# Kernel tuning notes

Hardware: AMD Instinct MI355X
Metric: run time of the kernel (lower is better)

## Reference

```python
import jax, jax.numpy as jnp
import numpy as np

N_NODES = 100000
N_EDGES = 3200000
IN_F = 256
OUT_F = 256
NEG_SLOPE = 0.2


def setup_inputs() -> dict:
    key = jax.random.key(0)
    ks = jax.random.split(key, 8)
    x = jax.random.normal(ks[0], (N_NODES, IN_F), dtype=jnp.float32)
    # linear_v: in_features -> out_features (W stored [in, out], y = x @ W + b)
    Wv = jax.random.normal(ks[1], (IN_F, OUT_F), dtype=jnp.float32) / np.sqrt(IN_F)
    bv = jnp.zeros((OUT_F,), dtype=jnp.float32)
    # linear_q / linear_k: out_features -> 1 (stored as vectors)
    wq = jax.random.normal(ks[2], (OUT_F,), dtype=jnp.float32) / np.sqrt(OUT_F)
    bq = jnp.zeros((), dtype=jnp.float32)
    wk = jax.random.normal(ks[3], (OUT_F,), dtype=jnp.float32) / np.sqrt(OUT_F)
    bk = jnp.zeros((), dtype=jnp.float32)
    src = jax.random.randint(ks[4], (N_EDGES,), 0, N_NODES, dtype=jnp.int32)
    dst = jax.random.randint(ks[5], (N_EDGES,), 0, N_NODES, dtype=jnp.int32)
    return {"x": x, "Wv": Wv, "bv": bv, "wq": wq, "bq": bq,
            "wk": wk, "bk": bk, "src": src, "dst": dst}


def reference(x, Wv, bv, wq, bq, wk, bk, src, dst):
    n = x.shape[0]
    h = x @ Wv + bv                      # [N, OUT_F] node values 'u'
    q = h @ wq + bq                      # [N] scalar per node
    k = h @ wk + bk                      # [N]
    e = q[src] + k[dst]                  # [E] u_add_v
    c = jnp.where(e > 0, e, NEG_SLOPE * e)  # leaky relu
    # edge softmax over incoming edges of each dst node (numerically stable)
    m = jax.ops.segment_max(c, dst, num_segments=n)   # [N]
    ex = jnp.exp(c - m[dst])                          # [E]
    s = jax.ops.segment_sum(ex, dst, num_segments=n)  # [N]
    attn = ex / s[dst]                                # [E]
    msg = h[src] * attn[:, None]                      # [E, OUT_F] u_mul_e
    out = jax.ops.segment_sum(msg, dst, num_segments=n)  # [N, OUT_F]
    return out
```

## Files before the change

kernel.cpp:

```cpp
#include <hip/hip_runtime.h>
#include <hip/hip_bf16.h>
#include <stdint.h>

#define NN 100000
#define NE 3200000
#define NPAD 100096
#define NB 391
#define CAPB 12288
#define SCAP 9216
#define GBLK 196
#define EPB 16384

typedef float  f32x4 __attribute__((ext_vector_type(4)));
typedef float  f32x2 __attribute__((ext_vector_type(2)));
typedef short  bf16x8 __attribute__((ext_vector_type(8)));
typedef int    i32x4 __attribute__((ext_vector_type(4)));

__device__ __forceinline__ float bf2f(unsigned short u){
  union { unsigned int i; float f; } v; v.i = ((unsigned int)u) << 16; return v.f;
}
__device__ __forceinline__ unsigned short f2bf(float f){
  __hip_bfloat16 b = __float2bfloat16(f);
  return __builtin_bit_cast(unsigned short, b);
}

__global__ __launch_bounds__(256) void k_prep_wvt(const float* __restrict__ Wv,
                                                  unsigned short* __restrict__ wvt){
  int n = blockIdx.x;
  int kp = threadIdx.x;
  int seg = kp >> 6, ct = (kp >> 3) & 7, o = kp & 7;
  int ks = (seg << 6) | ((ct ^ (n & 7)) << 3) | o;
  wvt[n * 256 + kp] = f2bf(Wv[ks * 256 + n]);
}

__global__ __launch_bounds__(256) void k_prep_vq(const float* __restrict__ Wv,
    const float* __restrict__ bv, const float* __restrict__ wq, const float* __restrict__ bq,
    const float* __restrict__ wk, const float* __restrict__ bk,
    float* __restrict__ vq, float* __restrict__ vk, float* __restrict__ consts){
  __shared__ float red[8];
  __shared__ float red2[8];
  int k = blockIdx.x, n = threadIdx.x;
  int wid = n >> 6, lane = n & 63;
  float w = Wv[k * 256 + n];
  float s1 = w * wq[n], s2 = w * wk[n];
  #pragma unroll
  for (int o = 32; o; o >>= 1){ s1 += __shfl_xor(s1, o, 64); s2 += __shfl_xor(s2, o, 64); }
  if (lane == 0){ red[wid] = s1; red[4 + wid] = s2; }
  __syncthreads();
  if (n == 0){ vq[k] = red[0]+red[1]+red[2]+red[3]; vk[k] = red[4]+red[5]+red[6]+red[7]; }
  if (k == 0){
    float t1 = bv[n] * wq[n], t2 = bv[n] * wk[n];
    #pragma unroll
    for (int o = 32; o; o >>= 1){ t1 += __shfl_xor(t1, o, 64); t2 += __shfl_xor(t2, o, 64); }
    if (lane == 0){ red2[wid] = t1; red2[4 + wid] = t2; }
    __syncthreads();
    if (n == 0){
      consts[0] = red2[0]+red2[1]+red2[2]+red2[3] + bq[0];
      consts[1] = red2[4]+red2[5]+red2[6]+red2[7] + bk[0];
    }
  }
}

__global__ __launch_bounds__(256) void k_convert_qk(const float* __restrict__ x,
    const float* __restrict__ vq, const float* __restrict__ vk, const float* __restrict__ consts,
    unsigned short* __restrict__ xs, float* __restrict__ q, float* __restrict__ kv){
  int row = (blockIdx.x * 256 + threadIdx.x) >> 6;
  int lane = threadIdx.x & 63;
  f32x4 xv = *(const f32x4*)(x + (size_t)row * 256 + lane * 4);
  f32x4 a  = *(const f32x4*)(vq + lane * 4);
  f32x4 b  = *(const f32x4*)(vk + lane * 4);
  float s1 = xv[0]*a[0] + xv[1]*a[1] + xv[2]*a[2] + xv[3]*a[3];
  float s2 = xv[0]*b[0] + xv[1]*b[1] + xv[2]*b[2] + xv[3]*b[3];
  ushort4 v4;
  v4.x = f2bf(xv[0]); v4.y = f2bf(xv[1]); v4.z = f2bf(xv[2]); v4.w = f2bf(xv[3]);
  int ct = ((lane >> 1) & 7) ^ (row & 7);
  char* dst = (char*)xs + (size_t)row * 512 + (lane >> 4) * 128 + ct * 16 + (lane & 1) * 8;
  *(ushort4*)dst = v4;
  #pragma unroll
  for (int o = 32; o; o >>= 1){ s1 += __shfl_xor(s1, o, 64); s2 += __shfl_xor(s2, o, 64); }
  if (lane == 0){ q[row] = s1 + consts[0]; kv[row] = s2 + consts[1]; }
}

__global__ __launch_bounds__(256) void k_gemm(const unsigned short* __restrict__ xs,
    const unsigned short* __restrict__ wvt, const float* __restrict__ bv,
    unsigned short* __restrict__ h){
  __shared__ unsigned short As[128 * 64];
  __shared__ unsigned short Bs[128 * 64];
  int bid = blockIdx.x;
  int bm = bid >> 1, bn = bid & 1;
  int tid = threadIdx.x, wid = tid >> 6, lane = tid & 63;
  int wr = wid >> 1, wc = wid & 1;
  f32x4 zero = {0.f, 0.f, 0.f, 0.f};
  f32x4 acc[4][4];
  #pragma unroll
  for (int i = 0; i < 4; i++)
    #pragma unroll
    for (int j = 0; j < 4; j++) acc[i][j] = zero;
  const char* gA0 = (const char*)xs  + (size_t)bm * 128 * 512;
  const char* gB0 = (const char*)wvt + (size_t)bn * 128 * 512;
  for (int k0b = 0; k0b < 512; k0b += 128){
    #pragma unroll
    for (int it = 0; it < 4; ++it){
      int base = (wid * 4 + it) * 1024;
      int loff = base + lane * 16;
      int row = loff >> 7, cb = loff & 127;
      __builtin_amdgcn_global_load_lds(
        (const __attribute__((address_space(1))) void*)(gA0 + (size_t)row * 512 + k0b + cb),
        (__attribute__((address_space(3))) void*)((char*)As + base), 16, 0, 0);
      __builtin_amdgcn_global_load_lds(
        (const __attribute__((address_space(1))) void*)(gB0 + (size_t)row * 512 + k0b + cb),
        (__attribute__((address_space(3))) void*)((char*)Bs + base), 16, 0, 0);
    }
    __syncthreads();
    #pragma unroll
    for (int kk = 0; kk < 2; ++kk){
      bf16x8 af[4], bfr[4];
      int cbase = kk * 4 + (lane >> 4);
      #pragma unroll
      for (int m = 0; m < 4; m++){
        int row = wr * 64 + m * 16 + (lane & 15);
        int c = cbase ^ (row & 7);
        af[m] = *(const bf16x8*)(As + row * 64 + c * 8);
      }
      #pragma unroll
      for (int n = 0; n < 4; n++){
        int col = wc * 64 + n * 16 + (lane & 15);
        int c = cbase ^ (col & 7);
        bfr[n] = *(const bf16x8*)(Bs + col * 64 + c * 8);
      }
      #pragma unroll
      for (int m = 0; m < 4; m++)
        #pragma unroll
        for (int n = 0; n < 4; n++)
          acc[m][n] = __builtin_amdgcn_mfma_f32_16x16x32_bf16(af[m], bfr[n], acc[m][n], 0, 0, 0);
    }
    __syncthreads();
  }
  unsigned short* hh = h + (size_t)bn * NPAD * 128;
  float bvv[4];
  #pragma unroll
  for (int n = 0; n < 4; n++) bvv[n] = bv[bn * 128 + wc * 64 + n * 16 + (lane & 15)];
  #pragma unroll
  for (int m = 0; m < 4; m++){
    int rowb = bm * 128 + wr * 64 + m * 16 + (lane >> 4) * 4;
    #pragma unroll
    for (int n = 0; n < 4; n++){
      int hcol = wc * 64 + n * 16 + (lane & 15);
      #pragma unroll
      for (int i = 0; i < 4; i++)
        hh[(size_t)(rowb + i) * 128 + hcol] = f2bf(acc[m][n][i] + bvv[n]);
    }
  }
}

__global__ __launch_bounds__(256) void k_group(const int* __restrict__ src,
    const int* __restrict__ dst, int* __restrict__ gTail, int* __restrict__ gReal,
    unsigned int* __restrict__ binned){
  __shared__ unsigned int   raw[EPB];
  __shared__ unsigned short rawB[EPB];
  __shared__ int cnt[NB];
  __shared__ int base[NB];
  __shared__ int cnt2[NB];
  int tid = threadIdx.x;
  for (int b = tid; b < NB; b += 256){ cnt[b] = 0; cnt2[b] = 0; }
  __syncthreads();
  int e0 = blockIdx.x * EPB;
  for (int r = 0; r < 16; ++r){
    int ebase = e0 + r * 1024 + tid * 4;
    int slot  = r * 1024 + tid * 4;
    uint4 vv; ushort4 bb4;
    if (ebase + 3 < NE){
      i32x4 s4 = __builtin_nontemporal_load((const i32x4*)(src + ebase));
      i32x4 d4 = __builtin_nontemporal_load((const i32x4*)(dst + ebase));
      #pragma unroll
      for (int j = 0; j < 4; j++){
        int d = d4[j]; int bkt = d >> 8;
        ((unsigned int*)&vv)[j] = ((unsigned)s4[j] << 8) | (unsigned)(d & 255);
        ((unsigned short*)&bb4)[j] = (unsigned short)bkt;
        atomicAdd(&cnt[bkt], 1);
      }
    } else {
      #pragma unroll
      for (int j = 0; j < 4; j++){
        int e = ebase + j;
        if (e < NE){
          int d = dst[e]; int s = src[e]; int bkt = d >> 8;
          ((unsigned int*)&vv)[j] = ((unsigned)s << 8) | (unsigned)(d & 255);
          ((unsigned short*)&bb4)[j] = (unsigned short)bkt;
          atomicAdd(&cnt[bkt], 1);
        } else {
          ((unsigned int*)&vv)[j] = 0xFFFFFFFFu;
          ((unsigned short*)&bb4)[j] = 0xFFFFu;
        }
      }
    }
    *(uint4*)(raw + slot) = vv;
    *(ushort4*)(rawB + slot) = bb4;
  }
  __syncthreads();
  for (int b = tid; b < NB; b += 256){
    int rr = cnt[b];
    int pr = (rr + 15) & ~15;
    int bs = atomicAdd(&gTail[b], pr);
    base[b] = bs;
    if (rr) atomicAdd(&gReal[b], rr);
    unsigned int* dp = binned + (size_t)b * CAPB;
    for (int k2 = rr; k2 < pr; ++k2){
      int p = bs + k2;
      if (p < CAPB) dp[p] = 0xFFFFFFFFu;
    }
  }
  __syncthreads();
  for (int r = 0; r < 16; ++r){
    int slot = r * 1024 + tid * 4;
    uint4 vv = *(const uint4*)(raw + slot);
    ushort4 bb4 = *(const ushort4*)(rawB + slot);
    #pragma unroll
    for (int j = 0; j < 4; j++){
      unsigned short bkt = ((unsigned short*)&bb4)[j];
      if (bkt != 0xFFFFu){
        int p = base[bkt] + atomicAdd(&cnt2[bkt], 1);
        if (p < CAPB) binned[(size_t)bkt * CAPB + p] = ((unsigned int*)&vv)[j];
      }
    }
  }
}

__global__ __launch_bounds__(256) void k_scanB(const int* __restrict__ gReal,
                                               int* __restrict__ bucketBase){
  __shared__ int sd[512];
  int tid = threadIdx.x;
  int v0 = tid < NB ? gReal[tid] : 0;
  int v1 = (tid + 256) < NB ? gReal[tid + 256] : 0;
  sd[tid] = v0; sd[tid + 256] = v1;
  __syncthreads();
  for (int o = 1; o < 512; o <<= 1){
    int t0 = (tid >= o) ? sd[tid - o] : 0;
    int t1 = (tid + 256 >= o) ? sd[tid + 256 - o] : 0;
    __syncthreads();
    sd[tid] += t0; sd[tid + 256] += t1;
    __syncthreads();
  }
  if (tid < NB) bucketBase[tid] = sd[tid] - v0;
  if (tid + 256 < NB) bucketBase[tid + 256] = sd[tid + 256] - v1;
}

__global__ __launch_bounds__(256) void k_sort(const unsigned int* __restrict__ binned,
    const int* __restrict__ gTail, const int* __restrict__ bucketBase,
    int* __restrict__ deg, int* __restrict__ rowStart, int* __restrict__ csrSrc){
  __shared__ int cnt[256], excl[256], cur[256];
  __shared__ int sorted[SCAP];
  int b = blockIdx.x, tid = threadIdx.x;
  int n = gTail[b]; if (n > CAPB) n = CAPB;
  int base = bucketBase[b];
  const unsigned int* L = binned + (size_t)b * CAPB;
  cnt[tid] = 0;
  __syncthreads();
  for (int i = tid; i < n; i += 256){
    unsigned int v = __builtin_nontemporal_load(L + i);
    if ((v >> 8) < NN) atomicAdd(&cnt[v & 255], 1);
  }
  __syncthreads();
  int myc = cnt[tid];
  excl[tid] = myc;
  __syncthreads();
  for (int o = 1; o < 256; o <<= 1){
    int t = (tid >= o) ? excl[tid - o] : 0;
    __syncthreads();
    excl[tid] += t;
    __syncthreads();
  }
  int ex = excl[tid] - myc;
  int node = b * 256 + tid;
  if (node < NN){ deg[node] = myc; rowStart[node] = base + ex; }
  cur[tid] = ex;
  __syncthreads();
  int m = excl[255];
  for (int i = tid; i < n; i += 256){
    unsigned int v = __builtin_nontemporal_load(L + i);
    unsigned int s = v >> 8;
    if (s < NN){
      int p = atomicAdd(&cur[v & 255], 1);
      if (p < SCAP) sorted[p] = (int)s;
    }
  }
  __syncthreads();
  for (int i = tid; i < m; i += 256)
    __builtin_nontemporal_store(sorted[i], csrSrc + base + i);
}

__global__ __launch_bounds__(256) void k_agg(const int* __restrict__ csrSrc,
    const int* __restrict__ rowStart, const int* __restrict__ deg,
    const float* __restrict__ q, const float* __restrict__ kv,
    const unsigned short* __restrict__ hh, float* __restrict__ outp){
  int w = (blockIdx.x * 256 + threadIdx.x) >> 6;
  int lane = threadIdx.x & 63;
  int start = rowStart[w], d = deg[w];
  float kd = kv[w];
  float a0 = 0.f, a1 = 0.f, ssum = 0.f;
  for (int bse = 0; bse < d; bse += 64){
    int cnt = min(64, d - bse);
    float ex = 0.f; int s = 0;
    if (lane < cnt){
      s = __builtin_nontemporal_load(csrSrc + start + bse + lane);
      float c = q[s] + kd;
      c = c > 0.f ? c : 0.2f * c;
      ex = __expf(c);
    }
    ssum += ex;
    for (int j0 = 0; j0 < cnt; j0 += 8){
      float wg[8]; ushort2 hv[8];
      #pragma unroll
      for (int jj = 0; jj < 8; jj++){
        int j = j0 + jj;
        wg[jj] = __shfl(ex, j, 64);
        int sj = __shfl(s, j, 64);
        hv[jj] = *(const ushort2*)(hh + (size_t)sj * 128 + lane * 2);
      }
      #pragma unroll
      for (int jj = 0; jj < 8; jj++){
        a0 += wg[jj] * bf2f(hv[jj].x);
        a1 += wg[jj] * bf2f(hv[jj].y);
      }
    }
  }
  #pragma unroll
  for (int o = 32; o; o >>= 1) ssum += __shfl_xor(ssum, o, 64);
  float inv = d > 0 ? 1.0f / ssum : 0.0f;
  f32x2 r; r[0] = a0 * inv; r[1] = a1 * inv;
  __builtin_nontemporal_store(r, (f32x2*)(outp + (size_t)w * 256 + lane * 2));
}

extern "C" void kernel_launch(void* const* d_in, const int* in_sizes, int n_in,
                              void* d_out, int out_size, void* d_ws, size_t ws_size,
                              hipStream_t stream){
  const float* x  = (const float*)d_in[0];
  const float* Wv = (const float*)d_in[1];
  const float* bv = (const float*)d_in[2];
  const float* wq = (const float*)d_in[3];
  const float* bq = (const float*)d_in[4];
  const float* wk = (const float*)d_in[5];
  const float* bk = (const float*)d_in[6];
  const int*   src = (const int*)d_in[7];
  const int*   dst = (const int*)d_in[8];
  float* out = (float*)d_out;

  char* ws = (char*)d_ws;
  size_t off = 0;
  auto alloc = [&](size_t bytes) -> char* {
    off = (off + 511) & ~(size_t)511;
    char* p = ws + off; off += bytes; return p;
  };
  unsigned short* h  = (unsigned short*)alloc((size_t)NPAD * 256 * 2);
  unsigned short* xs = (unsigned short*)alloc((size_t)NPAD * 256 * 2);
  unsigned int* binned = (unsigned int*)xs;
  int* csrSrc = (int*)((char*)xs + (size_t)NB * CAPB * 4);
  unsigned short* wvt  = (unsigned short*)alloc(256 * 256 * 2);
  float* vq     = (float*)alloc(256 * 4);
  float* vk     = (float*)alloc(256 * 4);
  float* consts = (float*)alloc(512);
  float* q      = (float*)alloc((size_t)NN * 4);
  float* kv     = (float*)alloc((size_t)NN * 4);
  int* deg      = (int*)alloc((size_t)NN * 4);
  int* rowStart = (int*)alloc((size_t)NN * 4);
  int* gTail    = (int*)alloc((size_t)NB * 4 * 2);
  int* gReal    = gTail + NB;
  int* bucketBase = (int*)alloc((size_t)NB * 4);

  (void)hipMemsetAsync(gTail, 0, (size_t)NB * 4 * 2, stream);
  k_prep_wvt<<<256, 256, 0, stream>>>(Wv, wvt);
  k_prep_vq<<<256, 256, 0, stream>>>(Wv, bv, wq, bq, wk, bk, vq, vk, consts);
  k_convert_qk<<<NN / 4, 256, 0, stream>>>(x, vq, vk, consts, xs, q, kv);
  k_gemm<<<(NPAD / 128) * 2, 256, 0, stream>>>(xs, wvt, bv, h);
  k_group<<<GBLK, 256, 0, stream>>>(src, dst, gTail, gReal, binned);
  k_scanB<<<1, 256, 0, stream>>>(gReal, bucketBase);
  k_sort<<<NB, 256, 0, stream>>>(binned, gTail, bucketBase, deg, rowStart, csrSrc);
  k_agg<<<NN / 4, 256, 0, stream>>>(csrSrc, rowStart, deg, q, kv, h, out);
  k_agg<<<NN / 4, 256, 0, stream>>>(csrSrc, rowStart, deg, q, kv,
                                    h + (size_t)NPAD * 128, out + 128);
}
```

Baseline: 515.4 us.

## Aggregate all 256 features in one pass and fold small kernels together

The h matrix is now stored as a single row-major [N,256] bf16 array instead of two 128-column halves. k_agg processes all 256 columns in one launch, with each lane loading 4 bf16 values and writing a float4, so the per-edge softmax weight work and the CSR/q reads happen once instead of twice. The two prep kernels are merged into one launch, and the bucket scan is recomputed redundantly inside each k_sort block, removing two launches. The trade-off is lower occupancy or memory-level parallelism per edge in k_agg, plus redundant scan work in every sort block.

```diff
diff --git a/kernel.cpp b/kernel.cpp
--- a/kernel.cpp
+++ b/kernel.cpp
@@ -12,34 +12,30 @@
 #define EPB 16384
 
 typedef float  f32x4 __attribute__((ext_vector_type(4)));
-typedef float  f32x2 __attribute__((ext_vector_type(2)));
 typedef short  bf16x8 __attribute__((ext_vector_type(8)));
 typedef int    i32x4 __attribute__((ext_vector_type(4)));
 
-__device__ __forceinline__ float bf2f(unsigned short u){
-  union { unsigned int i; float f; } v; v.i = ((unsigned int)u) << 16; return v.f;
-}
 __device__ __forceinline__ unsigned short f2bf(float f){
   __hip_bfloat16 b = __float2bfloat16(f);
   return __builtin_bit_cast(unsigned short, b);
 }
 
-__global__ __launch_bounds__(256) void k_prep_wvt(const float* __restrict__ Wv,
-                                                  unsigned short* __restrict__ wvt){
-  int n = blockIdx.x;
-  int kp = threadIdx.x;
-  int seg = kp >> 6, ct = (kp >> 3) & 7, o = kp & 7;
-  int ks = (seg << 6) | ((ct ^ (n & 7)) << 3) | o;
-  wvt[n * 256 + kp] = f2bf(Wv[ks * 256 + n]);
-}
-
-__global__ __launch_bounds__(256) void k_prep_vq(const float* __restrict__ Wv,
+__global__ __launch_bounds__(256) void k_prep(const float* __restrict__ Wv,
     const float* __restrict__ bv, const float* __restrict__ wq, const float* __restrict__ bq,
     const float* __restrict__ wk, const float* __restrict__ bk,
-    float* __restrict__ vq, float* __restrict__ vk, float* __restrict__ consts){
+    unsigned short* __restrict__ wvt, float* __restrict__ vq, float* __restrict__ vk,
+    float* __restrict__ consts){
   __shared__ float red[8];
   __shared__ float red2[8];
-  int k = blockIdx.x, n = threadIdx.x;
+  if (blockIdx.x < 256){
+    int n = blockIdx.x;
+    int kp = threadIdx.x;
+    int seg = kp >> 6, ct = (kp >> 3) & 7, o = kp & 7;
+    int ks = (seg << 6) | ((ct ^ (n & 7)) << 3) | o;
+    wvt[n * 256 + kp] = f2bf(Wv[ks * 256 + n]);
+    return;
+  }
+  int k = blockIdx.x - 256, n = threadIdx.x;
   int wid = n >> 6, lane = n & 63;
   float w = Wv[k * 256 + n];
   float s1 = w * wq[n], s2 = w * wk[n];
@@ -136,19 +132,19 @@
     }
     __syncthreads();
   }
-  unsigned short* hh = h + (size_t)bn * NPAD * 128;
+  int colb = bn * 128 + wc * 64;
   float bvv[4];
   #pragma unroll
-  for (int n = 0; n < 4; n++) bvv[n] = bv[bn * 128 + wc * 64 + n * 16 + (lane & 15)];
+  for (int n = 0; n < 4; n++) bvv[n] = bv[colb + n * 16 + (lane & 15)];
   #pragma unroll
   for (int m = 0; m < 4; m++){
     int rowb = bm * 128 + wr * 64 + m * 16 + (lane >> 4) * 4;
     #pragma unroll
     for (int n = 0; n < 4; n++){
-      int hcol = wc * 64 + n * 16 + (lane & 15);
+      int col = colb + n * 16 + (lane & 15);
       #pragma unroll
       for (int i = 0; i < 4; i++)
-        hh[(size_t)(rowb + i) * 128 + hcol] = f2bf(acc[m][n][i] + bvv[n]);
+        h[(size_t)(rowb + i) * 256 + col] = f2bf(acc[m][n][i] + bvv[n]);
     }
   }
 }
@@ -226,36 +222,28 @@
   }
 }
 
-__global__ __launch_bounds__(256) void k_scanB(const int* __restrict__ gReal,
-                                               int* __restrict__ bucketBase){
-  __shared__ int sd[512];
-  int tid = threadIdx.x;
-  int v0 = tid < NB ? gReal[tid] : 0;
-  int v1 = (tid + 256) < NB ? gReal[tid + 256] : 0;
-  sd[tid] = v0; sd[tid + 256] = v1;
-  __syncthreads();
-  for (int o = 1; o < 512; o <<= 1){
-    int t0 = (tid >= o) ? sd[tid - o] : 0;
-    int t1 = (tid + 256 >= o) ? sd[tid + 256 - o] : 0;
-    __syncthreads();
-    sd[tid] += t0; sd[tid + 256] += t1;
-    __syncthreads();
-  }
-  if (tid < NB) bucketBase[tid] = sd[tid] - v0;
-  if (tid + 256 < NB) bucketBase[tid + 256] = sd[tid + 256] - v1;
-}
-
 __global__ __launch_bounds__(256) void k_sort(const unsigned int* __restrict__ binned,
-    const int* __restrict__ gTail, const int* __restrict__ bucketBase,
+    const int* __restrict__ gTail, const int* __restrict__ gReal,
     int* __restrict__ deg, int* __restrict__ rowStart, int* __restrict__ csrSrc){
+  __shared__ int sg[512];
   __shared__ int cnt[256], excl[256], cur[256];
   __shared__ int sorted[SCAP];
   int b = blockIdx.x, tid = threadIdx.x;
+  int v0 = tid < NB ? gReal[tid] : 0;
+  int v1 = (tid + 256) < NB ? gReal[tid + 256] : 0;
+  sg[tid] = v0; sg[tid + 256] = v1;
+  cnt[tid] = 0;
+  __syncthreads();
+  for (int o = 1; o < 512; o <<= 1){
+    int t0 = (tid >= o) ? sg[tid - o] : 0;
+    int t1 = (tid + 256 >= o) ? sg[tid + 256 - o] : 0;
+    __syncthreads();
+    sg[tid] += t0; sg[tid + 256] += t1;
+    __syncthreads();
+  }
+  int base = (b == 0) ? 0 : sg[b - 1];
   int n = gTail[b]; if (n > CAPB) n = CAPB;
-  int base = bucketBase[b];
   const unsigned int* L = binned + (size_t)b * CAPB;
-  cnt[tid] = 0;
-  __syncthreads();
   for (int i = tid; i < n; i += 256){
     unsigned int v = __builtin_nontemporal_load(L + i);
     if ((v >> 8) < NN) atomicAdd(&cnt[v & 255], 1);
@@ -292,12 +280,12 @@
 __global__ __launch_bounds__(256) void k_agg(const int* __restrict__ csrSrc,
     const int* __restrict__ rowStart, const int* __restrict__ deg,
     const float* __restrict__ q, const float* __restrict__ kv,
-    const unsigned short* __restrict__ hh, float* __restrict__ outp){
+    const unsigned short* __restrict__ h, float* __restrict__ outp){
   int w = (blockIdx.x * 256 + threadIdx.x) >> 6;
   int lane = threadIdx.x & 63;
   int start = rowStart[w], d = deg[w];
   float kd = kv[w];
-  float a0 = 0.f, a1 = 0.f, ssum = 0.f;
+  float a0 = 0.f, a1 = 0.f, a2 = 0.f, a3 = 0.f, ssum = 0.f;
   for (int bse = 0; bse < d; bse += 64){
     int cnt = min(64, d - bse);
     float ex = 0.f; int s = 0;
@@ -309,26 +297,29 @@
     }
     ssum += ex;
     for (int j0 = 0; j0 < cnt; j0 += 8){
-      float wg[8]; ushort2 hv[8];
+      float wg[8]; uint2 hv[8];
       #pragma unroll
       for (int jj = 0; jj < 8; jj++){
         int j = j0 + jj;
         wg[jj] = __shfl(ex, j, 64);
         int sj = __shfl(s, j, 64);
-        hv[jj] = *(const ushort2*)(hh + (size_t)sj * 128 + lane * 2);
+        hv[jj] = *(const uint2*)(h + (size_t)sj * 256 + lane * 4);
       }
       #pragma unroll
       for (int jj = 0; jj < 8; jj++){
-        a0 += wg[jj] * bf2f(hv[jj].x);
-        a1 += wg[jj] * bf2f(hv[jj].y);
+        unsigned int u0 = hv[jj].x, u1 = hv[jj].y;
+        a0 += wg[jj] * __uint_as_float(u0 << 16);
+        a1 += wg[jj] * __uint_as_float(u0 & 0xFFFF0000u);
+        a2 += wg[jj] * __uint_as_float(u1 << 16);
+        a3 += wg[jj] * __uint_as_float(u1 & 0xFFFF0000u);
       }
     }
   }
   #pragma unroll
   for (int o = 32; o; o >>= 1) ssum += __shfl_xor(ssum, o, 64);
   float inv = d > 0 ? 1.0f / ssum : 0.0f;
-  f32x2 r; r[0] = a0 * inv; r[1] = a1 * inv;
-  __builtin_nontemporal_store(r, (f32x2*)(outp + (size_t)w * 256 + lane * 2));
+  f32x4 r; r[0] = a0 * inv; r[1] = a1 * inv; r[2] = a2 * inv; r[3] = a3 * inv;
+  __builtin_nontemporal_store(r, (f32x4*)(outp + (size_t)w * 256 + lane * 4));
 }
 
 extern "C" void kernel_launch(void* const* d_in, const int* in_sizes, int n_in,
@@ -365,17 +356,12 @@
   int* rowStart = (int*)alloc((size_t)NN * 4);
   int* gTail    = (int*)alloc((size_t)NB * 4 * 2);
   int* gReal    = gTail + NB;
-  int* bucketBase = (int*)alloc((size_t)NB * 4);
 
   (void)hipMemsetAsync(gTail, 0, (size_t)NB * 4 * 2, stream);
-  k_prep_wvt<<<256, 256, 0, stream>>>(Wv, wvt);
-  k_prep_vq<<<256, 256, 0, stream>>>(Wv, bv, wq, bq, wk, bk, vq, vk, consts);
+  k_prep<<<512, 256, 0, stream>>>(Wv, bv, wq, bq, wk, bk, wvt, vq, vk, consts);
   k_convert_qk<<<NN / 4, 256, 0, stream>>>(x, vq, vk, consts, xs, q, kv);
   k_gemm<<<(NPAD / 128) * 2, 256, 0, stream>>>(xs, wvt, bv, h);
   k_group<<<GBLK, 256, 0, stream>>>(src, dst, gTail, gReal, binned);
-  k_scanB<<<1, 256, 0, stream>>>(gReal, bucketBase);
-  k_sort<<<NB, 256, 0, stream>>>(binned, gTail, bucketBase, deg, rowStart, csrSrc);
+  k_sort<<<NB, 256, 0, stream>>>(binned, gTail, gReal, deg, rowStart, csrSrc);
   k_agg<<<NN / 4, 256, 0, stream>>>(csrSrc, rowStart, deg, q, kv, h, out);
-  k_agg<<<NN / 4, 256, 0, stream>>>(csrSrc, rowStart, deg, q, kv,
-                                    h + (size_t)NPAD * 128, out + 128);
-}
+}
```

New measurement: 520.7 us. No clear change (+1.0%).
